# Kernel tuning notes

Measured on AMD Instinct MI355X. Metric: run time of the kernel, lower is better.

## Reference

```python
import jax, jax.numpy as jnp
import numpy as np

B, S, D = 4, 2048, 1024

def setup_inputs() -> dict:
    key = jax.random.key(0)
    ks = jax.random.split(key, 7)
    scale = 1.0 / np.sqrt(D)
    return {
        "x": jax.random.normal(ks[0], (B, S, D), dtype=jnp.float32),
        "Wq": jax.random.normal(ks[1], (D, D), dtype=jnp.float32) * scale,
        "bq": jax.random.normal(ks[2], (D,), dtype=jnp.float32) * 0.01,
        "Wk": jax.random.normal(ks[3], (D, D), dtype=jnp.float32) * scale,
        "bk": jax.random.normal(ks[4], (D,), dtype=jnp.float32) * 0.01,
        "Wv": jax.random.normal(ks[5], (D, D), dtype=jnp.float32) * scale,
        "bv": jax.random.normal(ks[6], (D,), dtype=jnp.float32) * 0.01,
    }

def reference(x, Wq, bq, Wk, bk, Wv, bv):
    # Linear projections (torch Linear: x @ W^T + b; here W stored as [in,out])
    Q = jnp.einsum('bsd,de->bse', x, Wq) + bq
    K = jnp.einsum('bsd,de->bse', x, Wk) + bk
    V = jnp.einsum('bsd,de->bse', x, Wv) + bv
    scale = 1.0 / jnp.sqrt(jnp.asarray(Q.shape[-1], dtype=Q.dtype))
    scores = jnp.einsum('bqd,bkd->bqk', Q, K) * scale  # [B,S,S]
    attn = jax.nn.softmax(scores, axis=-1)
    return jnp.einsum('bqk,bkd->bqd', attn, V)
```

## Files before the change

kernel.cpp:

```cpp
#include <hip/hip_runtime.h>
#include <stdint.h>

#define BK 32

typedef __attribute__((ext_vector_type(8))) short bf16x8;
typedef __attribute__((ext_vector_type(4))) float f32x4;

__device__ __forceinline__ unsigned short f2bf(float f) {
  unsigned int u = __builtin_bit_cast(unsigned int, f);
  u += 0x7fffu + ((u >> 16) & 1u);
  return (unsigned short)(u >> 16);
}
__device__ __forceinline__ float bf2f(unsigned short h) {
  unsigned int u = ((unsigned int)h) << 16;
  return __builtin_bit_cast(float, u);
}

__device__ __forceinline__ void gll16(const void* g, void* l) {
  __builtin_amdgcn_global_load_lds(
      (const __attribute__((address_space(1))) unsigned int*)g,
      (__attribute__((address_space(3))) unsigned int*)l, 16, 0, 0);
}

template <int BIASMODE, int F32OUT>
__global__ __launch_bounds__(256) void bt_gemm(
    const unsigned short* __restrict__ A, const unsigned short* __restrict__ B,
    const float* __restrict__ bias, void* __restrict__ Cv,
    int M, int N, int K, int lda, int ldb, int ldc,
    long batchA, long batchB, long batchC, float scale) {
  __shared__ __align__(16) unsigned short As[128 * BK];
  __shared__ __align__(16) unsigned short Bs[128 * BK];

  const int z = blockIdx.z;
  A += (long)z * batchA;
  B += (long)z * batchB;

  const int tid = threadIdx.x;
  const int lane = tid & 63;
  const int wid = tid >> 6;
  const int wr = wid >> 1, wc = wid & 1;
  const int bm0 = blockIdx.y * 128;
  const int bn0 = blockIdx.x * 128;

  f32x4 zero = {0.f, 0.f, 0.f, 0.f};
  f32x4 acc[4][4];
#pragma unroll
  for (int m = 0; m < 4; m++)
#pragma unroll
    for (int n = 0; n < 4; n++) acc[m][n] = zero;

  const int nk = K / BK;
  for (int kt = 0; kt < nk; ++kt) {
    const int kk = kt * BK;
#pragma unroll
    for (int i = 0; i < 2; i++) {
      int c = tid + i * 256;
      int row = c >> 2, sub = c & 3;
      gll16(A + (size_t)(bm0 + row) * lda + kk + sub * 8, (void*)(As + c * 8));
      gll16(B + (size_t)(bn0 + row) * ldb + kk + sub * 8, (void*)(Bs + c * 8));
    }
    __syncthreads();

    const int kq = (lane >> 4) * 8;
    bf16x8 af[4], bfr[4];
#pragma unroll
    for (int m = 0; m < 4; m++) {
      int r = wr * 64 + m * 16 + (lane & 15);
      af[m] = *(const bf16x8*)&As[r * BK + kq];
    }
#pragma unroll
    for (int n = 0; n < 4; n++) {
      int cidx = wc * 64 + n * 16 + (lane & 15);
      bfr[n] = *(const bf16x8*)&Bs[cidx * BK + kq];
    }
#pragma unroll
    for (int m = 0; m < 4; m++)
#pragma unroll
      for (int n = 0; n < 4; n++)
        acc[m][n] = __builtin_amdgcn_mfma_f32_16x16x32_bf16(af[m], bfr[n],
                                                            acc[m][n], 0, 0, 0);
    __syncthreads();
  }

  float* Cf = (float*)Cv + (F32OUT ? (long)z * batchC : 0);
  unsigned short* Cb = (unsigned short*)Cv + (F32OUT ? 0 : (long)z * batchC);
#pragma unroll
  for (int m = 0; m < 4; m++) {
    int row0 = bm0 + wr * 64 + m * 16 + ((lane >> 4) << 2);
#pragma unroll
    for (int n = 0; n < 4; n++) {
      int col = bn0 + wc * 64 + n * 16 + (lane & 15);
      f32x4 v = acc[m][n];
      float bc = (BIASMODE == 1) ? bias[col] : 0.0f;
#pragma unroll
      for (int j = 0; j < 4; j++) {
        float bj = (BIASMODE == 2) ? bias[row0 + j] : bc;
        float r = v[j] * scale + bj;
        if (F32OUT)
          Cf[(size_t)(row0 + j) * ldc + col] = r;
        else
          Cb[(size_t)(row0 + j) * ldc + col] = f2bf(r);
      }
    }
  }
}

__global__ __launch_bounds__(256) void cvt_kernel(const float* __restrict__ in,
                                                  unsigned short* __restrict__ out,
                                                  long n4) {
  long i = (long)blockIdx.x * blockDim.x + threadIdx.x;
  long stride = (long)gridDim.x * blockDim.x;
  for (; i < n4; i += stride) {
    float4 f = ((const float4*)in)[i];
    uint2 w;
    w.x = (unsigned int)f2bf(f.x) | ((unsigned int)f2bf(f.y) << 16);
    w.y = (unsigned int)f2bf(f.z) | ((unsigned int)f2bf(f.w) << 16);
    ((uint2*)out)[i] = w;
  }
}

__global__ __launch_bounds__(1024) void transposeW_kernel(
    const float* __restrict__ W, unsigned short* __restrict__ Wt) {
  __shared__ float t[32][33];
  int x = threadIdx.x, y = threadIdx.y;
  int d = blockIdx.y * 32 + y, n = blockIdx.x * 32 + x;
  t[y][x] = W[(size_t)d * 1024 + n];
  __syncthreads();
  int nn = blockIdx.x * 32 + y, dd = blockIdx.y * 32 + x;
  Wt[(size_t)nn * 1024 + dd] = f2bf(t[x][y]);
}

__global__ __launch_bounds__(256) void softmax_kernel(unsigned short* __restrict__ SP) {
  const int row = blockIdx.x;
  unsigned short* rp = SP + (size_t)row * 2048;
  const int tid = threadIdx.x;
  const int wid = tid >> 6, lane = tid & 63;

  uint4 u = ((const uint4*)rp)[tid];
  float xv[8];
  xv[0] = bf2f(u.x & 0xffff); xv[1] = bf2f(u.x >> 16);
  xv[2] = bf2f(u.y & 0xffff); xv[3] = bf2f(u.y >> 16);
  xv[4] = bf2f(u.z & 0xffff); xv[5] = bf2f(u.z >> 16);
  xv[6] = bf2f(u.w & 0xffff); xv[7] = bf2f(u.w >> 16);

  float m = xv[0];
#pragma unroll
  for (int j = 1; j < 8; j++) m = fmaxf(m, xv[j]);
#pragma unroll
  for (int off = 32; off >= 1; off >>= 1) m = fmaxf(m, __shfl_xor(m, off));

  __shared__ float redm[4];
  __shared__ float reds[4];
  if (lane == 0) redm[wid] = m;
  __syncthreads();
  m = fmaxf(fmaxf(redm[0], redm[1]), fmaxf(redm[2], redm[3]));

  float p[8], s = 0.f;
#pragma unroll
  for (int j = 0; j < 8; j++) {
    p[j] = __expf(xv[j] - m);
    s += p[j];
  }
#pragma unroll
  for (int off = 32; off >= 1; off >>= 1) s += __shfl_xor(s, off);
  if (lane == 0) reds[wid] = s;
  __syncthreads();
  float inv = 1.0f / (reds[0] + reds[1] + reds[2] + reds[3]);

  uint4 o;
  o.x = (unsigned int)f2bf(p[0] * inv) | ((unsigned int)f2bf(p[1] * inv) << 16);
  o.y = (unsigned int)f2bf(p[2] * inv) | ((unsigned int)f2bf(p[3] * inv) << 16);
  o.z = (unsigned int)f2bf(p[4] * inv) | ((unsigned int)f2bf(p[5] * inv) << 16);
  o.w = (unsigned int)f2bf(p[6] * inv) | ((unsigned int)f2bf(p[7] * inv) << 16);
  ((uint4*)rp)[tid] = o;
}

extern "C" void kernel_launch(void* const* d_in, const int* in_sizes, int n_in,
                              void* d_out, int out_size, void* d_ws, size_t ws_size,
                              hipStream_t stream) {
  const float* x = (const float*)d_in[0];
  const float* Wq = (const float*)d_in[1];
  const float* bq = (const float*)d_in[2];
  const float* Wk = (const float*)d_in[3];
  const float* bk = (const float*)d_in[4];
  const float* Wv = (const float*)d_in[5];
  const float* bv = (const float*)d_in[6];
  float* out = (float*)d_out;

  char* ws = (char*)d_ws;
  unsigned short* xb = (unsigned short*)ws;
  unsigned short* Kb = (unsigned short*)(ws + (16L << 20));
  unsigned short* Vt = (unsigned short*)(ws + (32L << 20));
  unsigned short* Qb = (unsigned short*)(ws + (48L << 20));
  unsigned short* Wtq = (unsigned short*)(ws + (64L << 20));
  unsigned short* Wtk = Wtq + 1024 * 1024;
  unsigned short* Wtv = Wtk + 1024 * 1024;
  unsigned short* SP = (unsigned short*)(ws + (70L << 20));

  cvt_kernel<<<2048, 256, 0, stream>>>(x, xb, 2097152L);

  dim3 tb(32, 32);
  transposeW_kernel<<<dim3(32, 32), tb, 0, stream>>>(Wq, Wtq);
  transposeW_kernel<<<dim3(32, 32), tb, 0, stream>>>(Wk, Wtk);
  transposeW_kernel<<<dim3(32, 32), tb, 0, stream>>>(Wv, Wtv);

  bt_gemm<1, 0><<<dim3(8, 64, 1), 256, 0, stream>>>(
      xb, Wtq, bq, Qb, 8192, 1024, 1024, 1024, 1024, 1024, 0, 0, 0, 1.0f);
  bt_gemm<1, 0><<<dim3(8, 64, 1), 256, 0, stream>>>(
      xb, Wtk, bk, Kb, 8192, 1024, 1024, 1024, 1024, 1024, 0, 0, 0, 1.0f);

  bt_gemm<2, 0><<<dim3(16, 8, 4), 256, 0, stream>>>(
      Wtv, xb, bv, Vt, 1024, 2048, 1024, 1024, 1024, 2048,
      0, 2048L * 1024, 1024L * 2048, 1.0f);

  bt_gemm<0, 0><<<dim3(16, 16, 4), 256, 0, stream>>>(
      Qb, Kb, nullptr, SP, 2048, 2048, 1024, 1024, 1024, 2048,
      2048L * 1024, 2048L * 1024, 2048L * 2048, 0.03125f);

  softmax_kernel<<<8192, 256, 0, stream>>>(SP);

  bt_gemm<0, 1><<<dim3(8, 16, 4), 256, 0, stream>>>(
      SP, Vt, nullptr, out, 2048, 1024, 2048, 2048, 2048, 1024,
      2048L * 2048, 1024L * 2048, 2048L * 1024, 1.0f);
}
```

Baseline: 325.4 us.

## Replace GEMM with 256x256 double-buffered swizzled-LDS kernel and fuse QK projection

```diff
diff --git a/kernel.cpp b/kernel.cpp
--- a/kernel.cpp
+++ b/kernel.cpp
@@ -1,7 +1,5 @@
 #include <hip/hip_runtime.h>
 #include <stdint.h>
-
-#define BK 32
 
 typedef __attribute__((ext_vector_type(8))) short bf16x8;
 typedef __attribute__((ext_vector_type(4))) float f32x4;
@@ -22,84 +20,196 @@
       (__attribute__((address_space(3))) unsigned int*)l, 16, 0, 0);
 }
 
+#define SB() __builtin_amdgcn_sched_barrier(0)
+#define BAR() __builtin_amdgcn_s_barrier()
+#define VMC6()                                     \
+  asm volatile("s_waitcnt vmcnt(6)" ::: "memory"); \
+  __builtin_amdgcn_sched_barrier(0)
+
+__device__ __forceinline__ void stage2(const unsigned short* src, int ld,
+                                       int rowbase, int kt, char* lds,
+                                       int opofs, int dbuf, int half, int tid) {
+#pragma unroll
+  for (int i = 0; i < 2; i++) {
+    int c = tid + i * 512;
+    int r7 = c >> 3, ch = c & 7;
+    int sch = ch ^ (r7 & 7);
+    const char* g =
+        (const char*)(src + (size_t)(rowbase + half * 128 + r7) * ld) +
+        kt * 128 + sch * 16;
+    gll16(g, lds + opofs + (dbuf * 2 + half) * 16384 + c * 16);
+  }
+}
+
+__device__ __forceinline__ void ld_ahalf(const char* lds, int d, int mh, int wr,
+                                         int lane, bf16x8 a[4][2]) {
+#pragma unroll
+  for (int m = 0; m < 4; m++)
+#pragma unroll
+    for (int kk = 0; kk < 2; kk++) {
+      int r7 = wr * 64 + m * 16 + (lane & 15);
+      int c = ((lane >> 4) + kk * 4) ^ (lane & 7);
+      a[m][kk] =
+          *(const bf16x8*)(lds + (d * 2 + mh) * 16384 + r7 * 128 + c * 16);
+    }
+}
+__device__ __forceinline__ void ld_bhalf(const char* lds, int d, int nh, int wc,
+                                         int lane, bf16x8 b[2][2]) {
+#pragma unroll
+  for (int n = 0; n < 2; n++)
+#pragma unroll
+    for (int kk = 0; kk < 2; kk++) {
+      int r7 = wc * 32 + n * 16 + (lane & 15);
+      int c = ((lane >> 4) + kk * 4) ^ (lane & 7);
+      b[n][kk] = *(const bf16x8*)(lds + 65536 + (d * 2 + nh) * 16384 +
+                                  r7 * 128 + c * 16);
+    }
+}
+
+template <int MH, int NH>
+__device__ __forceinline__ void mfma16(f32x4 acc[8][4], const bf16x8 a[4][2],
+                                       const bf16x8 b[2][2]) {
+  __builtin_amdgcn_s_setprio(1);
+#pragma unroll
+  for (int m = 0; m < 4; m++)
+#pragma unroll
+    for (int n = 0; n < 2; n++)
+#pragma unroll
+      for (int kk = 0; kk < 2; kk++)
+        acc[MH * 4 + m][NH * 2 + n] = __builtin_amdgcn_mfma_f32_16x16x32_bf16(
+            a[m][kk], b[n][kk], acc[MH * 4 + m][NH * 2 + n], 0, 0, 0);
+  __builtin_amdgcn_s_setprio(0);
+}
+
 template <int BIASMODE, int F32OUT>
-__global__ __launch_bounds__(256) void bt_gemm(
+__global__ __launch_bounds__(512, 2) void gemm8(
     const unsigned short* __restrict__ A, const unsigned short* __restrict__ B,
-    const float* __restrict__ bias, void* __restrict__ Cv,
-    int M, int N, int K, int lda, int ldb, int ldc,
-    long batchA, long batchB, long batchC, float scale) {
-  __shared__ __align__(16) unsigned short As[128 * BK];
-  __shared__ __align__(16) unsigned short Bs[128 * BK];
-
+    const float* __restrict__ bias1, const float* __restrict__ bias2,
+    void* __restrict__ Cv, int K, int lda, int ldb, int ldc, long batchA,
+    long batchB, long batchC, float scale) {
+  extern __shared__ char lds[];
   const int z = blockIdx.z;
   A += (long)z * batchA;
   B += (long)z * batchB;
 
+  const int gx = gridDim.x;
+  const int nwg = gx * gridDim.y;
+  const int lin = blockIdx.y * gx + blockIdx.x;
+  const int s = (lin & 7) * (nwg >> 3) + (lin >> 3);
+  const int bn0 = (s % gx) * 256;
+  const int bm0 = (s / gx) * 256;
+
   const int tid = threadIdx.x;
   const int lane = tid & 63;
   const int wid = tid >> 6;
-  const int wr = wid >> 1, wc = wid & 1;
-  const int bm0 = blockIdx.y * 128;
-  const int bn0 = blockIdx.x * 128;
-
-  f32x4 zero = {0.f, 0.f, 0.f, 0.f};
-  f32x4 acc[4][4];
-#pragma unroll
-  for (int m = 0; m < 4; m++)
-#pragma unroll
-    for (int n = 0; n < 4; n++) acc[m][n] = zero;
-
-  const int nk = K / BK;
-  for (int kt = 0; kt < nk; ++kt) {
-    const int kk = kt * BK;
-#pragma unroll
-    for (int i = 0; i < 2; i++) {
-      int c = tid + i * 256;
-      int row = c >> 2, sub = c & 3;
-      gll16(A + (size_t)(bm0 + row) * lda + kk + sub * 8, (void*)(As + c * 8));
-      gll16(B + (size_t)(bn0 + row) * ldb + kk + sub * 8, (void*)(Bs + c * 8));
-    }
-    __syncthreads();
-
-    const int kq = (lane >> 4) * 8;
-    bf16x8 af[4], bfr[4];
-#pragma unroll
-    for (int m = 0; m < 4; m++) {
-      int r = wr * 64 + m * 16 + (lane & 15);
-      af[m] = *(const bf16x8*)&As[r * BK + kq];
-    }
-#pragma unroll
-    for (int n = 0; n < 4; n++) {
-      int cidx = wc * 64 + n * 16 + (lane & 15);
-      bfr[n] = *(const bf16x8*)&Bs[cidx * BK + kq];
-    }
-#pragma unroll
-    for (int m = 0; m < 4; m++)
-#pragma unroll
-      for (int n = 0; n < 4; n++)
-        acc[m][n] = __builtin_amdgcn_mfma_f32_16x16x32_bf16(af[m], bfr[n],
-                                                            acc[m][n], 0, 0, 0);
-    __syncthreads();
-  }
-
+  const int wr = wid >> 2, wc = wid & 3;
+
+  f32x4 acc[8][4];
+#pragma unroll
+  for (int i = 0; i < 8; i++)
+#pragma unroll
+    for (int j = 0; j < 4; j++) acc[i][j] = (f32x4){0.f, 0.f, 0.f, 0.f};
+
+  const int nkt = K >> 6;
+  const int niter = nkt >> 1;
+
+  stage2(A, lda, bm0, 0, lds, 0, 0, 0, tid);
+  stage2(B, ldb, bn0, 0, lds, 65536, 0, 0, tid);
+  stage2(A, lda, bm0, 0, lds, 0, 0, 1, tid);
+  stage2(B, ldb, bn0, 0, lds, 65536, 0, 1, tid);
+  stage2(A, lda, bm0, 1, lds, 0, 1, 0, tid);
+  stage2(B, ldb, bn0, 1, lds, 65536, 1, 0, tid);
+  stage2(A, lda, bm0, 1, lds, 0, 1, 1, tid);
+  VMC6();
+  BAR();
+
+  bf16x8 a[2][4][2], b[2][2][2];
+  for (int it = 0; it < niter; ++it) {
+    const int t1 = 2 * it + 1;
+    int t2 = 2 * it + 2;
+    if (t2 >= nkt) t2 = nkt - 1;
+    int t3 = 2 * it + 3;
+    if (t3 >= nkt) t3 = nkt - 1;
+
+    ld_ahalf(lds, 0, 0, wr, lane, a[0]);
+    ld_bhalf(lds, 0, 0, wc, lane, b[0]);
+    stage2(B, ldb, bn0, t1, lds, 65536, 1, 1, tid);
+    SB();
+    BAR();
+    mfma16<0, 0>(acc, a[0], b[0]);
+    SB();
+    BAR();
+    ld_ahalf(lds, 0, 1, wr, lane, a[1]);
+    stage2(A, lda, bm0, t2, lds, 0, 0, 0, tid);
+    SB();
+    BAR();
+    mfma16<1, 0>(acc, a[1], b[0]);
+    SB();
+    BAR();
+    ld_bhalf(lds, 0, 1, wc, lane, b[1]);
+    stage2(B, ldb, bn0, t2, lds, 65536, 0, 0, tid);
+    SB();
+    BAR();
+    mfma16<0, 1>(acc, a[0], b[1]);
+    SB();
+    BAR();
+    stage2(A, lda, bm0, t2, lds, 0, 0, 1, tid);
+    VMC6();
+    BAR();
+    mfma16<1, 1>(acc, a[1], b[1]);
+    SB();
+    BAR();
+    ld_ahalf(lds, 1, 0, wr, lane, a[0]);
+    ld_bhalf(lds, 1, 0, wc, lane, b[0]);
+    stage2(B, ldb, bn0, t2, lds, 65536, 0, 1, tid);
+    SB();
+    BAR();
+    mfma16<0, 0>(acc, a[0], b[0]);
+    SB();
+    BAR();
+    ld_ahalf(lds, 1, 1, wr, lane, a[1]);
+    stage2(A, lda, bm0, t3, lds, 0, 1, 0, tid);
+    SB();
+    BAR();
+    mfma16<1, 0>(acc, a[1], b[0]);
+    SB();
+    BAR();
+    ld_bhalf(lds, 1, 1, wc, lane, b[1]);
+    stage2(B, ldb, bn0, t3, lds, 65536, 1, 0, tid);
+    SB();
+    BAR();
+    mfma16<0, 1>(acc, a[0], b[1]);
+    SB();
+    BAR();
+    stage2(A, lda, bm0, t3, lds, 0, 1, 1, tid);
+    VMC6();
+    BAR();
+    mfma16<1, 1>(acc, a[1], b[1]);
+    SB();
+    BAR();
+  }
+
+  const int r4 = (lane >> 4) << 2;
+  const int c0 = lane & 15;
   float* Cf = (float*)Cv + (F32OUT ? (long)z * batchC : 0);
   unsigned short* Cb = (unsigned short*)Cv + (F32OUT ? 0 : (long)z * batchC);
 #pragma unroll
-  for (int m = 0; m < 4; m++) {
-    int row0 = bm0 + wr * 64 + m * 16 + ((lane >> 4) << 2);
-#pragma unroll
-    for (int n = 0; n < 4; n++) {
-      int col = bn0 + wc * 64 + n * 16 + (lane & 15);
-      f32x4 v = acc[m][n];
-      float bc = (BIASMODE == 1) ? bias[col] : 0.0f;
+  for (int am = 0; am < 8; am++) {
+    int row = bm0 + (am >> 2) * 128 + wr * 64 + (am & 3) * 16 + r4;
+#pragma unroll
+    for (int an = 0; an < 4; an++) {
+      int col = bn0 + (an >> 1) * 128 + wc * 32 + (an & 1) * 16 + c0;
+      float bc = 0.f;
+      if (BIASMODE == 1) bc = (col < 1024) ? bias1[col] : bias2[col - 1024];
+      f32x4 v = acc[am][an];
 #pragma unroll
       for (int j = 0; j < 4; j++) {
-        float bj = (BIASMODE == 2) ? bias[row0 + j] : bc;
+        float bj = (BIASMODE == 2) ? bias1[row + j] : bc;
         float r = v[j] * scale + bj;
         if (F32OUT)
-          Cf[(size_t)(row0 + j) * ldc + col] = r;
+          Cf[(size_t)(row + j) * ldc + col] = r;
         else
-          Cb[(size_t)(row0 + j) * ldc + col] = f2bf(r);
+          Cb[(size_t)(row + j) * ldc + col] = f2bf(r);
       }
     }
   }
@@ -155,15 +265,15 @@
   __syncthreads();
   m = fmaxf(fmaxf(redm[0], redm[1]), fmaxf(redm[2], redm[3]));
 
-  float p[8], s = 0.f;
+  float p[8], sm = 0.f;
 #pragma unroll
   for (int j = 0; j < 8; j++) {
     p[j] = __expf(xv[j] - m);
-    s += p[j];
-  }
-#pragma unroll
-  for (int off = 32; off >= 1; off >>= 1) s += __shfl_xor(s, off);
-  if (lane == 0) reds[wid] = s;
+    sm += p[j];
+  }
+#pragma unroll
+  for (int off = 32; off >= 1; off >>= 1) sm += __shfl_xor(sm, off);
+  if (lane == 0) reds[wid] = sm;
   __syncthreads();
   float inv = 1.0f / (reds[0] + reds[1] + reds[2] + reds[3]);
 
@@ -189,13 +299,22 @@
 
   char* ws = (char*)d_ws;
   unsigned short* xb = (unsigned short*)ws;
-  unsigned short* Kb = (unsigned short*)(ws + (16L << 20));
-  unsigned short* Vt = (unsigned short*)(ws + (32L << 20));
-  unsigned short* Qb = (unsigned short*)(ws + (48L << 20));
-  unsigned short* Wtq = (unsigned short*)(ws + (64L << 20));
+  unsigned short* QKb = (unsigned short*)(ws + (16L << 20));
+  unsigned short* Vt = (unsigned short*)(ws + (48L << 20));
+  unsigned short* SP = (unsigned short*)(ws + (64L << 20));
+  unsigned short* Wtq = (unsigned short*)(ws + (96L << 20));
   unsigned short* Wtk = Wtq + 1024 * 1024;
   unsigned short* Wtv = Wtk + 1024 * 1024;
-  unsigned short* SP = (unsigned short*)(ws + (70L << 20));
+
+  const int LDS8 = 131072;
+  (void)hipFuncSetAttribute(reinterpret_cast<const void*>(&gemm8<1, 0>),
+                            hipFuncAttributeMaxDynamicSharedMemorySize, LDS8);
+  (void)hipFuncSetAttribute(reinterpret_cast<const void*>(&gemm8<2, 0>),
+                            hipFuncAttributeMaxDynamicSharedMemorySize, LDS8);
+  (void)hipFuncSetAttribute(reinterpret_cast<const void*>(&gemm8<0, 0>),
+                            hipFuncAttributeMaxDynamicSharedMemorySize, LDS8);
+  (void)hipFuncSetAttribute(reinterpret_cast<const void*>(&gemm8<0, 1>),
+                            hipFuncAttributeMaxDynamicSharedMemorySize, LDS8);
 
   cvt_kernel<<<2048, 256, 0, stream>>>(x, xb, 2097152L);
 
@@ -204,22 +323,19 @@
   transposeW_kernel<<<dim3(32, 32), tb, 0, stream>>>(Wk, Wtk);
   transposeW_kernel<<<dim3(32, 32), tb, 0, stream>>>(Wv, Wtv);
 
-  bt_gemm<1, 0><<<dim3(8, 64, 1), 256, 0, stream>>>(
-      xb, Wtq, bq, Qb, 8192, 1024, 1024, 1024, 1024, 1024, 0, 0, 0, 1.0f);
-  bt_gemm<1, 0><<<dim3(8, 64, 1), 256, 0, stream>>>(
-      xb, Wtk, bk, Kb, 8192, 1024, 1024, 1024, 1024, 1024, 0, 0, 0, 1.0f);
-
-  bt_gemm<2, 0><<<dim3(16, 8, 4), 256, 0, stream>>>(
-      Wtv, xb, bv, Vt, 1024, 2048, 1024, 1024, 1024, 2048,
-      0, 2048L * 1024, 1024L * 2048, 1.0f);
-
-  bt_gemm<0, 0><<<dim3(16, 16, 4), 256, 0, stream>>>(
-      Qb, Kb, nullptr, SP, 2048, 2048, 1024, 1024, 1024, 2048,
-      2048L * 1024, 2048L * 1024, 2048L * 2048, 0.03125f);
+  gemm8<1, 0><<<dim3(8, 32, 1), 512, LDS8, stream>>>(
+      xb, Wtq, bq, bk, QKb, 1024, 1024, 1024, 2048, 0, 0, 0, 1.0f);
+
+  gemm8<2, 0><<<dim3(32, 4, 1), 512, LDS8, stream>>>(
+      Wtv, xb, bv, nullptr, Vt, 1024, 1024, 1024, 8192, 0, 0, 0, 1.0f);
+
+  gemm8<0, 0><<<dim3(8, 8, 4), 512, LDS8, stream>>>(
+      QKb, QKb + 1024, nullptr, nullptr, SP, 1024, 2048, 2048, 2048,
+      2048L * 2048, 2048L * 2048, 2048L * 2048, 0.03125f);
 
   softmax_kernel<<<8192, 256, 0, stream>>>(SP);
 
-  bt_gemm<0, 1><<<dim3(8, 16, 4), 256, 0, stream>>>(
-      SP, Vt, nullptr, out, 2048, 1024, 2048, 2048, 2048, 1024,
-      2048L * 2048, 1024L * 2048, 2048L * 1024, 1.0f);
-}
+  gemm8<0, 1><<<dim3(4, 8, 4), 512, LDS8, stream>>>(
+      SP, Vt, nullptr, nullptr, out, 2048, 2048, 8192, 1024, 2048L * 2048,
+      2048L, 2048L * 1024, 1.0f);
+}
```

Measured after the change: 285.7 us. 1.14x faster.
